# Kernel optimization log

Hardware: AMD Instinct MI355X
Metric: run time of the kernel (lower is better)

## Reference

```python
import jax, jax.numpy as jnp
import numpy as np

B = 8
RESOLUTIONS = [65, 129, 257, 513, 1025]
NUM_POINTS = [0, 4096, 16384, 65536, 262144]
CLIP_MIN = -1e9
FINAL = 1025          # last resolution (both axes)
B_MIN, B_MAX = -1.0, 1.0
BALANCE = 0.5


def setup_inputs() -> dict:
    key = jax.random.key(0)
    k1, k2, k3, k4 = jax.random.split(key, 4)
    return {
        "w1": jax.random.normal(k1, (2, 256), jnp.float32),
        "b1": jax.random.normal(k2, (256,), jnp.float32),
        "w2": jax.random.normal(k3, (256, 1), jnp.float32),
        "b2": jax.random.normal(k4, (1,), jnp.float32),
    }


def _interp_bilinear_ac(x, H, W):
    """F.interpolate(..., mode='bilinear', align_corners=True). x: [B, C, h, w]."""
    b, c, h, w = x.shape
    ys = jnp.linspace(0.0, h - 1.0, H)
    xs = jnp.linspace(0.0, w - 1.0, W)
    y0 = jnp.floor(ys).astype(jnp.int32)
    y1 = jnp.minimum(y0 + 1, h - 1)
    wy = ys - y0
    x0 = jnp.floor(xs).astype(jnp.int32)
    x1 = jnp.minimum(x0 + 1, w - 1)
    wx = xs - x0
    # interpolate rows, then columns
    top = x[:, :, y0, :] * (1.0 - wy)[None, None, :, None] + x[:, :, y1, :] * wy[None, None, :, None]
    return top[:, :, :, x0] * (1.0 - wx) + top[:, :, :, x1] * wx


def _batch_eval(coords, w1, b1, w2, b2):
    """coords: [B, N, 2] in final-resolution pixel space (align_corners=False mapping).
    Returns occupancy [B, N] (C == 1)."""
    coords2d = coords / FINAL + 0.5 / FINAL                 # normalize to [0, 1]
    p = coords2d * (B_MAX - B_MIN) + B_MIN                  # [B, N, 2] in world coords
    h = jax.nn.relu(jnp.einsum('bnd,dh->bnh', p, w1) + b1)  # [B, N, 256]
    occ = jax.nn.sigmoid(jnp.einsum('bnh,ho->bno', h, w2) + b2)
    return occ[..., 0]


def reference(w1, b1, w2, b2):
    occ = None
    for i, res in enumerate(RESOLUTIONS):
        if i == 0:
            # init_coords: grid of res x res points spanning [0, FINAL-1]
            xs = jnp.linspace(0.0, FINAL - 1.0, res)
            gy, gx = jnp.meshgrid(xs, xs, indexing='ij')          # y rows, x cols
            coords = jnp.stack([gx.ravel(), gy.ravel()], axis=-1)  # [N, 2] (x, y)
            coords = jnp.broadcast_to(coords, (B, res * res, 2))
            o = _batch_eval(coords, w1, b1, w2, b2)               # [B, N]
            occ = o.reshape(B, 1, res, res)                       # [B, C, H, W]
        else:
            occ = _interp_bilinear_ac(occ, res, res)
            npt = NUM_POINTS[i]
            if npt <= 0:
                continue
            # uncertainty = -|occ - balance_value|
            unc = -jnp.abs(occ - BALANCE)                          # [B, 1, H, W]
            flat_unc = unc.reshape(B, res * res)
            scores, idx = jax.lax.top_k(flat_unc, npt)             # [B, npt]
            px = (idx % res).astype(jnp.float32)
            py = (idx // res).astype(jnp.float32)
            stride = (FINAL - 1.0) / (res - 1.0)
            coords = jnp.stack([px, py], axis=-1) * stride         # [B, npt, 2]
            new_vals = _batch_eval(coords, w1, b1, w2, b2)         # [B, npt]
            occ_flat = occ.reshape(B, res * res)
            old_vals = jnp.take_along_axis(occ_flat, idx, axis=1)
            vals = jnp.where(scores >= CLIP_MIN, new_vals, old_vals)
            occ_flat = jax.vmap(lambda o, i2, v: o.at[i2].set(v))(occ_flat, idx, vals)
            occ = occ_flat.reshape(B, 1, res, res)
    return occ
```

## Files before the change

kernel.cpp:

```cpp
#include <hip/hip_runtime.h>
#include <stdint.h>

#define HID 256
#define NMAXPIX (1025 * 1025)
#define NREP 8
#define NSEG 2048
#define SELMAX 2112

#define HISTA_OFF 0
#define HISTB_OFF 16384
#define HISTC_OFF 32768
#define SCAL_OFF  40960
#define TIC_OFF   41024
#define STAGE_U32 43072

#define R1P 65
#define R1  129
#define N1  (129 * 129)
#define NPT1 4096u
#define NSEG1 256
#define SEG1 66
#define B1 64
#define NREP1 4

__device__ __forceinline__ uint32_t aload(const uint32_t* p) {
    return __hip_atomic_load(p, __ATOMIC_RELAXED, __HIP_MEMORY_SCOPE_AGENT);
}
__device__ __forceinline__ void astore(uint32_t* p, uint32_t v) {
    __hip_atomic_store(p, v, __ATOMIC_RELAXED, __HIP_MEMORY_SCOPE_AGENT);
}

__device__ __forceinline__ float mlp_eval4(float wx, float wy,
                                           const float4* __restrict__ w1x,
                                           const float4* __restrict__ w1y,
                                           const float4* __restrict__ vb1,
                                           const float4* __restrict__ vw2, float b2v) {
    const float C0 = (float)(0.5 / 1025.0);
    float px = (wx / 1025.0f + C0) * 2.0f - 1.0f;
    float py = (wy / 1025.0f + C0) * 2.0f - 1.0f;
    float a0 = 0.f, a1 = 0.f, a2 = 0.f, a3 = 0.f;
#pragma unroll 8
    for (int q = 0; q < HID / 4; ++q) {
        float4 a = w1x[q], b = w1y[q], c = vb1[q], d = vw2[q];
        float h0 = px * a.x + py * b.x + c.x;
        float h1 = px * a.y + py * b.y + c.y;
        float h2 = px * a.z + py * b.z + c.z;
        float h3 = px * a.w + py * b.w + c.w;
        h0 = h0 > 0.f ? h0 : 0.f;
        h1 = h1 > 0.f ? h1 : 0.f;
        h2 = h2 > 0.f ? h2 : 0.f;
        h3 = h3 > 0.f ? h3 : 0.f;
        a0 += h0 * d.x;
        a1 += h1 * d.y;
        a2 += h2 * d.z;
        a3 += h3 * d.w;
    }
    float x = ((a0 + a1) + (a2 + a3)) + b2v;
    float r;
    if (x >= 0.f) { r = 1.0f / (1.0f + expf(-x)); }
    else { float e = expf(x); r = e / (1.0f + e); }
    return r;
}

__device__ __forceinline__ uint32_t block_exscan_256(uint32_t v, volatile uint32_t* lds4) {
    int lane = threadIdx.x & 63, w = threadIdx.x >> 6;
    uint32_t inc = v;
#pragma unroll
    for (int d = 1; d < 64; d <<= 1) {
        uint32_t o = (uint32_t)__shfl_up((int)inc, d, 64);
        if (lane >= d) inc += o;
    }
    if (lane == 63) lds4[w] = inc;
    __syncthreads();
    uint32_t woff = 0;
    for (int i = 0; i < w; ++i) woff += lds4[i];
    return woff + inc - v;
}

__device__ void scan_generic(const uint32_t* __restrict__ hist, int NB, int nrep,
                             uint32_t rem_in, uint32_t prefix_in, int shift,
                             uint32_t* outp, uint32_t* outr,
                             volatile uint32_t* lds4, volatile uint32_t* ldspair) {
    int tid = threadIdx.x;
    int C = NB >> 8;
    int b0 = NB - (tid + 1) * C;
    uint32_t cnts[8];
#pragma unroll
    for (int k = 0; k < 8; ++k) cnts[k] = 0;
    for (int rep = 0; rep < nrep; ++rep) {
        const uint4* p = (const uint4*)(hist + (size_t)rep * NB + b0);
#pragma unroll
        for (int g = 0; g < 2; ++g) {
            if (g * 4 < C) {
                uint4 v = p[g];
                cnts[g * 4 + 0] += v.x;
                cnts[g * 4 + 1] += v.y;
                cnts[g * 4 + 2] += v.z;
                cnts[g * 4 + 3] += v.w;
            }
        }
    }
    uint32_t ssum = 0;
    for (int k = 0; k < C; ++k) ssum += cnts[k];
    uint32_t excl = block_exscan_256(ssum, lds4);
    uint32_t run = excl;
    for (int k = 0; k < C; ++k) {
        uint32_t c = cnts[C - 1 - k];
        if (rem_in > run && rem_in <= run + c) {
            ldspair[0] = (prefix_in << shift) | (uint32_t)(b0 + C - 1 - k);
            ldspair[1] = rem_in - run;
        }
        run += c;
    }
    __syncthreads();
    *outp = ldspair[0];
    *outr = ldspair[1];
}

__device__ void scan_atomic(const uint32_t* __restrict__ hist, int NB, int nrep,
                            uint32_t rem_in, uint32_t prefix_in, int shift,
                            uint32_t* outp, uint32_t* outr,
                            volatile uint32_t* lds4, volatile uint32_t* ldspair) {
    int tid = threadIdx.x;
    int C = NB >> 8;
    int b0 = NB - (tid + 1) * C;
    uint32_t cnts[8];
#pragma unroll
    for (int k = 0; k < 8; ++k) cnts[k] = 0;
    for (int rep = 0; rep < nrep; ++rep)
        for (int k = 0; k < C; ++k)
            cnts[k] += aload(&hist[(size_t)rep * NB + b0 + k]);
    uint32_t ssum = 0;
    for (int k = 0; k < C; ++k) ssum += cnts[k];
    uint32_t excl = block_exscan_256(ssum, lds4);
    uint32_t run = excl;
    for (int k = 0; k < C; ++k) {
        uint32_t c = cnts[C - 1 - k];
        if (rem_in > run && rem_in <= run + c) {
            ldspair[0] = (prefix_in << shift) | (uint32_t)(b0 + C - 1 - k);
            ldspair[1] = rem_in - run;
        }
        run += c;
    }
    __syncthreads();
    *outp = ldspair[0];
    *outr = ldspair[1];
}

__device__ __forceinline__ void hist_add(uint32_t* lh, uint32_t bin, bool act, int lane) {
    unsigned long long m = __ballot(act);
    if (m) {
        int leader = __ffsll(m) - 1;
        uint32_t lbin = (uint32_t)__shfl((int)bin, leader, 64);
        unsigned long long smk = __ballot(act && bin == lbin);
        if (smk == m) {
            if (lane == leader) atomicAdd(&lh[lbin], (uint32_t)__popcll(m));
        } else if (act) {
            atomicAdd(&lh[bin], 1u);
        }
    }
}

__device__ __forceinline__ float up2x(const float* __restrict__ in, int rp, int r, int n) {
    int i = n / r, j = n % r;
    int i2 = i >> 1, j2 = j >> 1;
    float v;
    if ((i & 1) == 0) {
        if ((j & 1) == 0) {
            v = in[i2 * rp + j2];
        } else {
            float a = in[i2 * rp + j2], b = in[i2 * rp + j2 + 1];
            v = a * 0.5f + b * 0.5f;
        }
    } else {
        if ((j & 1) == 0) {
            float a = in[i2 * rp + j2], b = in[(i2 + 1) * rp + j2];
            v = a * 0.5f + b * 0.5f;
        } else {
            float a = in[i2 * rp + j2],      c = in[i2 * rp + j2 + 1];
            float b = in[(i2 + 1) * rp + j2], d = in[(i2 + 1) * rp + j2 + 1];
            float t1 = a * 0.5f + b * 0.5f;
            float t2 = c * 0.5f + d * 0.5f;
            v = t1 * 0.5f + t2 * 0.5f;
        }
    }
    return v;
}

__device__ __forceinline__ uint32_t mkkey(float v) {
    float unc = -fabsf(v - 0.5f);
    uint32_t u = __float_as_uint(unc);
    return (u & 0x80000000u) ? ~u : (u | 0x80000000u);
}

__device__ __forceinline__ uint32_t key_of(const float* __restrict__ in, int rp, int r, int n) {
    return mkkey(up2x(in, rp, r, n));
}

__device__ bool wait_ctr(uint32_t* ctr, uint32_t target, volatile uint32_t* sflag) {
    if (threadIdx.x == 0) {
        uint32_t d = aload(ctr);
        int sp = 0;
        while (d < target && sp < 20000) {
            __builtin_amdgcn_s_sleep(4);
            d = aload(ctr);
            ++sp;
        }
        *sflag = (d >= target) ? 1u : 0u;
    }
    __syncthreads();
    return *sflag != 0;
}

__global__ __launch_bounds__(256) void k_eval0z(const float* __restrict__ w1, const float* __restrict__ b1,
                                                const float* __restrict__ w2, const float* __restrict__ b2,
                                                float* __restrict__ occ, uint32_t* __restrict__ zbuf, int zcount) {
    __shared__ alignas(16) float sw1[2 * HID];
    __shared__ alignas(16) float sb1[HID];
    __shared__ alignas(16) float sw2[HID];
    int tid = threadIdx.x;
    for (int i = tid; i < 2 * HID; i += 256) sw1[i] = w1[i];
    sb1[tid] = b1[tid];
    sw2[tid] = w2[tid];
    __syncthreads();
    int gtid = blockIdx.x * 256 + tid;
    int nthreads = gridDim.x * 256;
    for (int i = gtid; i < zcount; i += nthreads) zbuf[i] = 0;
    for (int n = gtid; n < 65 * 65; n += nthreads) {
        int i = n / 65, j = n % 65;
        occ[n] = mlp_eval4(16.0f * (float)j, 16.0f * (float)i,
                           (const float4*)sw1, (const float4*)(sw1 + HID),
                           (const float4*)sb1, (const float4*)sw2, b2[0]);
    }
}

__global__ __launch_bounds__(256) void k_s1all(const float* __restrict__ in,
                                               float* __restrict__ outg,
                                               uint32_t* __restrict__ keys,
                                               uint32_t* __restrict__ sm,
                                               const float* __restrict__ w1, const float* __restrict__ b1,
                                               const float* __restrict__ w2, const float* __restrict__ b2) {
    __shared__ alignas(16) float sw1[2 * HID];
    __shared__ alignas(16) float sb1[HID];
    __shared__ alignas(16) float sw2[HID];
    __shared__ alignas(16) uint32_t lh[2048];
    __shared__ uint32_t selidx[SELMAX];
    __shared__ uint32_t selcnt;
    __shared__ uint32_t lds4[4];
    __shared__ uint32_t ldspair[2];
    __shared__ uint32_t sflag;

    uint32_t* histA = sm + HISTA_OFF;
    uint32_t* histB = sm + HISTB_OFF;
    uint32_t* histC = sm + HISTC_OFF;
    uint32_t* scal  = sm + SCAL_OFF;
    uint32_t* tic   = sm + TIC_OFF;

    const int tid = threadIdx.x, lane = tid & 63, w = tid >> 6;
    for (int i = tid; i < 2 * HID; i += 256) sw1[i] = w1[i];
    sb1[tid] = b1[tid];
    sw2[tid] = w2[tid];
    if (tid == 0) selcnt = 0;
    for (int k = tid; k < 2048; k += 256) lh[k] = 0;
    __syncthreads();

    for (int n0 = blockIdx.x * 256; n0 < N1; n0 += B1 * 256) {
        int n = n0 + tid;
        bool act = n < N1;
        uint32_t key = 0;
        if (act) {
            float v = up2x(in, R1P, R1, n);
            outg[n] = v;
            key = mkkey(v);
            astore(&keys[n], key);
        }
        hist_add(lh, key >> 21, act, lane);
    }
    __syncthreads();
    {
        uint32_t* rep = histA + (size_t)(blockIdx.x & (NREP1 - 1)) * 2048;
        for (int k = tid; k < 2048; k += 256) { uint32_t c = lh[k]; if (c) atomicAdd(&rep[k], c); }
    }
    __syncthreads();
    if (tid == 0) __hip_atomic_fetch_add(&scal[8], 1u, __ATOMIC_RELAXED, __HIP_MEMORY_SCOPE_AGENT);

    uint32_t pfx1, rem1;
    if (wait_ctr(&scal[8], B1, &sflag)) {
        scan_atomic(histA, 2048, NREP1, NPT1, 0u, 0, &pfx1, &rem1, lds4, ldspair);
    } else {
        for (int k = tid; k < 2048; k += 256) lh[k] = 0;
        __syncthreads();
        for (int n0 = 0; n0 < N1; n0 += 256) {
            int n = n0 + tid; bool act = n < N1;
            uint32_t key = act ? key_of(in, R1P, R1, n) : 0u;
            hist_add(lh, key >> 21, act, lane);
        }
        __syncthreads();
        scan_generic(lh, 2048, 1, NPT1, 0u, 0, &pfx1, &rem1, lds4, ldspair);
    }

    for (int k = tid; k < 2048; k += 256) lh[k] = 0;
    __syncthreads();
    for (int n0 = blockIdx.x * 256; n0 < N1; n0 += B1 * 256) {
        int n = n0 + tid;
        bool act = n < N1;
        uint32_t key = act ? aload(&keys[n]) : 0u;
        bool flt = act && ((key >> 21) == pfx1);
        hist_add(lh, (key >> 10) & 0x7FFu, flt, lane);
    }
    __syncthreads();
    {
        uint32_t* rep = histB + (size_t)(blockIdx.x & (NREP1 - 1)) * 2048;
        for (int k = tid; k < 2048; k += 256) { uint32_t c = lh[k]; if (c) atomicAdd(&rep[k], c); }
    }
    __syncthreads();
    if (tid == 0) __hip_atomic_fetch_add(&scal[9], 1u, __ATOMIC_RELAXED, __HIP_MEMORY_SCOPE_AGENT);

    uint32_t pfx2, rem2;
    if (wait_ctr(&scal[9], B1, &sflag)) {
        scan_atomic(histB, 2048, NREP1, rem1, pfx1, 11, &pfx2, &rem2, lds4, ldspair);
    } else {
        for (int k = tid; k < 2048; k += 256) lh[k] = 0;
        __syncthreads();
        for (int n0 = 0; n0 < N1; n0 += 256) {
            int n = n0 + tid; bool act = n < N1;
            uint32_t key = act ? key_of(in, R1P, R1, n) : 0u;
            bool flt = act && ((key >> 21) == pfx1);
            hist_add(lh, (key >> 10) & 0x7FFu, flt, lane);
        }
        __syncthreads();
        scan_generic(lh, 2048, 1, rem1, pfx1, 11, &pfx2, &rem2, lds4, ldspair);
    }

    for (int k = tid; k < 2048; k += 256) lh[k] = 0;
    __syncthreads();
    for (int n0 = blockIdx.x * 256; n0 < N1; n0 += B1 * 256) {
        int n = n0 + tid;
        bool act = n < N1;
        uint32_t key = act ? aload(&keys[n]) : 0u;
        bool flt = act && ((key >> 10) == pfx2);
        hist_add(lh, key & 0x3FFu, flt, lane);
    }
    __syncthreads();
    {
        uint32_t* rep = histC + (size_t)(blockIdx.x & (NREP1 - 1)) * 1024;
        for (int k = tid; k < 1024; k += 256) { uint32_t c = lh[k]; if (c) atomicAdd(&rep[k], c); }
    }
    __syncthreads();
    if (tid == 0) __hip_atomic_fetch_add(&scal[10], 1u, __ATOMIC_RELAXED, __HIP_MEMORY_SCOPE_AGENT);

    uint32_t K, t;
    if (wait_ctr(&scal[10], B1, &sflag)) {
        scan_atomic(histC, 1024, NREP1, rem2, pfx2, 10, &K, &t, lds4, ldspair);
    } else {
        for (int k = tid; k < 2048; k += 256) lh[k] = 0;
        __syncthreads();
        for (int n0 = 0; n0 < N1; n0 += 256) {
            int n = n0 + tid; bool act = n < N1;
            uint32_t key = act ? key_of(in, R1P, R1, n) : 0u;
            bool flt = act && ((key >> 10) == pfx2);
            hist_add(lh, key & 0x3FFu, flt, lane);
        }
        __syncthreads();
        scan_generic(lh, 1024, 1, rem2, pfx2, 10, &K, &t, lds4, ldspair);
    }

    int wv = blockIdx.x * 4 + w;
    int s0 = wv * SEG1;
    int s1e = s0 + SEG1; if (s1e > N1) s1e = N1;
    uint32_t tcnt = 0;
    for (int base = s0; base < s1e; base += 64) {
        int n = base + lane;
        if (n < s1e) tcnt += (aload(&keys[n]) == K) ? 1u : 0u;
    }
#pragma unroll
    for (int d = 32; d; d >>= 1) tcnt += (uint32_t)__shfl_down((int)tcnt, d, 64);
    if (lane == 0) astore(&tic[wv], tcnt);
    __syncthreads();
    if (tid == 0) __hip_atomic_fetch_add(&scal[11], 1u, __ATOMIC_RELAXED, __HIP_MEMORY_SCOPE_AGENT);

    uint32_t tp = 0;
    if (wait_ctr(&scal[11], B1, &sflag)) {
        for (int i = lane; i < wv; i += 64) tp += aload(&tic[i]);
    } else {
        for (int i = lane; i < wv; i += 64) {
            int a0 = i * SEG1, a1 = a0 + SEG1; if (a1 > N1) a1 = N1;
            uint32_t c = 0;
            for (int n2 = a0; n2 < a1; ++n2) c += (key_of(in, R1P, R1, n2) == K) ? 1u : 0u;
            tp += c;
        }
    }
#pragma unroll
    for (int d = 32; d; d >>= 1) tp += (uint32_t)__shfl_down((int)tp, d, 64);
    tp = (uint32_t)__shfl((int)tp, 0, 64);

    uint32_t tie_run = tp;
    unsigned long long lowmask = (lane == 63) ? ~0ull >> 1 : ((1ull << lane) - 1ull);
    for (int base = s0; base < s1e; base += 64) {
        int n = base + lane;
        bool inb = n < s1e;
        uint32_t key = inb ? aload(&keys[n]) : 0u;
        bool gt = inb && (key > K);
        bool tie = inb && (key == K);
        unsigned long long tm = __ballot(tie);
        uint32_t trank = tie_run + (uint32_t)__popcll(tm & lowmask);
        bool sel = gt || (tie && trank < t);
        unsigned long long smk = __ballot(sel);
        if (smk) {
            int leader = __ffsll(smk) - 1;
            uint32_t wbase = 0;
            if (lane == leader) wbase = atomicAdd(&selcnt, (uint32_t)__popcll(smk));
            wbase = (uint32_t)__shfl((int)wbase, leader, 64);
            if (sel) selidx[wbase + (uint32_t)__popcll(smk & lowmask)] = (uint32_t)n;
        }
        tie_run += (uint32_t)__popcll(tm);
    }
    __syncthreads();

    uint32_t cnt = selcnt;
    float vb2 = b2[0];
    for (uint32_t i = tid; i < cnt; i += 256) {
        int n = (int)selidx[i];
        int ii = n / R1, jj = n % R1;
        float rr = mlp_eval4(8.0f * (float)jj, 8.0f * (float)ii,
                             (const float4*)sw1, (const float4*)(sw1 + HID),
                             (const float4*)sb1, (const float4*)sw2, vb2);
        outg[n] = rr;
    }
}

__global__ __launch_bounds__(256) void k_upkey(const float* __restrict__ in, int rp,
                                               float* __restrict__ outg, int r, int nb, int bstride,
                                               uint32_t* __restrict__ keys,
                                               uint32_t* __restrict__ histA) {
    __shared__ uint32_t hist[2048];
    int tid = threadIdx.x;
    for (int k = tid; k < 2048; k += 256) hist[k] = 0;
    __syncthreads();
    int N = r * r;
    int lane = tid & 63;
    int gstride = gridDim.x * 256;
    for (int n0 = blockIdx.x * 256; n0 < N; n0 += gstride) {
        int n = n0 + tid;
        bool act = n < N;
        uint32_t key = 0;
        if (act) {
            float v = up2x(in, rp, r, n);
            for (int k = 0; k < nb; ++k) outg[(size_t)k * bstride + n] = v;
            key = mkkey(v);
            keys[n] = key;
        }
        hist_add(hist, key >> 21, act, lane);
    }
    __syncthreads();
    uint32_t* myrep = histA + (size_t)(blockIdx.x & (NREP - 1)) * 2048;
    for (int k = tid; k < 2048; k += 256) {
        uint32_t c = hist[k];
        if (c) atomicAdd(&myrep[k], c);
    }
}

__global__ __launch_bounds__(256) void k_histmid(const uint32_t* __restrict__ keys, int N,
                                                 const uint32_t* __restrict__ prevHist,
                                                 uint32_t* __restrict__ scal,
                                                 int useNpt, uint32_t npt, int scalInIdx, int shift,
                                                 int scalOutIdx,
                                                 int fshift, int bshift, uint32_t bmask,
                                                 uint32_t* __restrict__ outHist, int NBout) {
    __shared__ uint32_t lh[2048];
    __shared__ uint32_t lds4[4];
    __shared__ uint32_t ldspair[2];
    int tid = threadIdx.x, lane = tid & 63;
    uint32_t rem_in = useNpt ? npt : scal[scalInIdx + 1];
    uint32_t pfx_in = useNpt ? 0u  : scal[scalInIdx];
    uint32_t pfx, rem;
    scan_generic(prevHist, 2048, NREP, rem_in, pfx_in, shift, &pfx, &rem, lds4, ldspair);
    if (blockIdx.x == 0 && tid == 0) { scal[scalOutIdx] = pfx; scal[scalOutIdx + 1] = rem; }
    for (int k = tid; k < 2048; k += 256) lh[k] = 0;
    __syncthreads();
    int gstride = gridDim.x * 256;
    for (int base = blockIdx.x * 256; base < N; base += gstride) {
        int n = base + tid;
        bool inb = n < N;
        uint32_t key = inb ? keys[n] : 0u;
        bool flt = inb && ((key >> fshift) == pfx);
        uint32_t bin = (key >> bshift) & bmask;
        hist_add(lh, bin, flt, lane);
    }
    __syncthreads();
    uint32_t* myrep = outHist + (size_t)(blockIdx.x & (NREP - 1)) * NBout;
    for (int k = tid; k < NBout; k += 256) {
        uint32_t c = lh[k];
        if (c) atomicAdd(&myrep[k], c);
    }
}

__global__ __launch_bounds__(256, 2) void k_segselc(
        const uint32_t* __restrict__ keys, int N, int seglen,
        const uint32_t* __restrict__ histC,
        const uint32_t* __restrict__ scal,
        uint32_t* __restrict__ tic,
        uint32_t* __restrict__ gcnt,
        uint32_t* __restrict__ selbuf) {
    __shared__ uint32_t selcnt;
    __shared__ uint32_t selidx[SELMAX];
    __shared__ uint32_t lds4[4];
    __shared__ uint32_t ldspair[2];
    __shared__ uint32_t wtc[4];
    __shared__ uint32_t s_excl;
    __shared__ uint32_t gbase;
    int tid = threadIdx.x, lane = tid & 63, w = tid >> 6;
    if (tid == 0) { selcnt = 0; s_excl = 0; }

    uint32_t rem2 = scal[3], pfx2 = scal[2];
    uint32_t K, t;
    scan_generic(histC, 1024, NREP, rem2, pfx2, 10, &K, &t, lds4, ldspair);

    int wv = blockIdx.x * 4 + w;
    int s0 = wv * seglen;
    int s1 = s0 + seglen; if (s1 > N) s1 = N;
    uint32_t tcnt = 0;
    for (int base = s0; base < s1; base += 64) {
        int n = base + lane;
        if (n < s1) tcnt += (keys[n] == K) ? 1u : 0u;
    }
#pragma unroll
    for (int d = 32; d; d >>= 1) tcnt += (uint32_t)__shfl_down((int)tcnt, d, 64);
    if (lane == 0) wtc[w] = tcnt;
    __syncthreads();
    uint32_t agg = wtc[0] + wtc[1] + wtc[2] + wtc[3];
    uint32_t intra = 0;
    for (int i = 0; i < w; ++i) intra += wtc[i];

    if (tid == 0) {
        uint32_t st = (blockIdx.x == 0) ? ((2u << 30) | agg) : ((1u << 30) | agg);
        astore(&tic[blockIdx.x], st);
    }
    if (blockIdx.x > 0 && w == 0) {
        uint32_t excl = 0;
        int b = (int)blockIdx.x - 1;
        for (;;) {
            int mine = b - lane;
            bool active = (mine >= 0);
            uint32_t f = 0;
            if (active) {
                f = aload(&tic[mine]);
                int spins = 0;
                while ((f >> 30) == 0u && spins < 1000) {
                    __builtin_amdgcn_s_sleep(2);
                    f = aload(&tic[mine]);
                    ++spins;
                }
                if ((f >> 30) == 0u) {
                    int ms0 = mine * seglen;
                    int ms1 = ms0 + seglen; if (ms1 > N) ms1 = N;
                    uint32_t c = 0;
                    for (int n2 = ms0; n2 < ms1; ++n2) c += (keys[n2] == K) ? 1u : 0u;
                    f = (1u << 30) | c;
                }
            }
            unsigned long long incm = __ballot(active && (f >> 30) == 2u);
            uint32_t val;
            bool done = (incm != 0ull);
            if (done) {
                int l2 = __ffsll(incm) - 1;
                val = (lane <= l2) ? (f & 0x3FFFFFFFu) : 0u;
            } else {
                val = active ? (f & 0x3FFFFFFFu) : 0u;
            }
#pragma unroll
            for (int d = 32; d; d >>= 1) val += (uint32_t)__shfl_down((int)val, d, 64);
            val = (uint32_t)__shfl((int)val, 0, 64);
            excl += val;
            if (done) break;
            if (b < 64) break;
            b -= 64;
        }
        if (lane == 0) {
            astore(&tic[blockIdx.x], (2u << 30) | (excl + agg));
            s_excl = excl;
        }
    }
    __syncthreads();
    uint32_t tie_run = s_excl + intra;

    unsigned long long lowmask = (lane == 63) ? ~0ull >> 1 : ((1ull << lane) - 1ull);
    for (int base = s0; base < s1; base += 64) {
        int n = base + lane;
        bool inb = n < s1;
        uint32_t key = inb ? keys[n] : 0u;
        bool gt = inb && (key > K);
        bool tie = inb && (key == K);
        unsigned long long tm = __ballot(tie);
        uint32_t trank = tie_run + (uint32_t)__popcll(tm & lowmask);
        bool sel = gt || (tie && trank < t);
        unsigned long long smk = __ballot(sel);
        if (smk) {
            int leader = __ffsll(smk) - 1;
            uint32_t wbase = 0;
            if (lane == leader) wbase = atomicAdd(&selcnt, (uint32_t)__popcll(smk));
            wbase = (uint32_t)__shfl((int)wbase, leader, 64);
            if (sel) selidx[wbase + (uint32_t)__popcll(smk & lowmask)] = (uint32_t)n;
        }
        tie_run += (uint32_t)__popcll(tm);
    }
    __syncthreads();

    if (tid == 0) gbase = atomicAdd(gcnt, selcnt);
    __syncthreads();
    uint32_t cnt = selcnt, gb = gbase;
    for (uint32_t i = tid; i < cnt; i += 256) selbuf[gb + i] = selidx[i];
}

__global__ __launch_bounds__(256) void k_evalsel(const uint32_t* __restrict__ selbuf, int npt,
                                                 int r, float stride,
                                                 float* __restrict__ occ, int nb, int bstride,
                                                 const float* __restrict__ w1, const float* __restrict__ b1,
                                                 const float* __restrict__ w2, const float* __restrict__ b2) {
    __shared__ alignas(16) float sw1[2 * HID];
    __shared__ alignas(16) float sb1[HID];
    __shared__ alignas(16) float sw2[HID];
    int tid = threadIdx.x;
    for (int i = tid; i < 2 * HID; i += 256) sw1[i] = w1[i];
    sb1[tid] = b1[tid];
    sw2[tid] = w2[tid];
    __syncthreads();
    float vb2 = b2[0];
    int gs = gridDim.x * 256;
    for (int i = blockIdx.x * 256 + tid; i < npt; i += gs) {
        int n = (int)selbuf[i];
        int ii = n / r, jj = n % r;
        float rr = mlp_eval4(stride * (float)jj, stride * (float)ii,
                             (const float4*)sw1, (const float4*)(sw1 + HID),
                             (const float4*)sb1, (const float4*)sw2, vb2);
        for (int k = 0; k < nb; ++k) occ[(size_t)k * bstride + n] = rr;
    }
}

__global__ __launch_bounds__(256) void k_bcast(const float* __restrict__ src, float* __restrict__ dst, int N) {
    int q = blockIdx.x * 256 + threadIdx.x;
    int n = q * 4;
    if (n + 3 < N) {
        float4 v = *(const float4*)(src + n);
#pragma unroll
        for (int k = 0; k < 8; ++k) *(float4*)(dst + (size_t)k * N + n) = v;
    } else if (n < N) {
        for (int m = n; m < N; ++m) {
            float v = src[m];
#pragma unroll
            for (int k = 0; k < 8; ++k) dst[(size_t)k * N + m] = v;
        }
    }
}

extern "C" void kernel_launch(void* const* d_in, const int* in_sizes, int n_in,
                              void* d_out, int out_size, void* d_ws, size_t ws_size,
                              hipStream_t stream) {
    const float* w1 = (const float*)d_in[0];
    const float* b1 = (const float*)d_in[1];
    const float* w2 = (const float*)d_in[2];
    const float* b2 = (const float*)d_in[3];
    float* out = (float*)d_out;

    const size_t A = (((size_t)NMAXPIX * 4) + 255) & ~(size_t)255;
    const size_t SMALL_BYTES = (size_t)4 * STAGE_U32 * 4;
    const size_t SELB_BYTES = ((size_t)262144 * 4 + 255) & ~(size_t)255;
    const size_t need = 3 * A + SMALL_BYTES + SELB_BYTES;

    int fused8 = (ws_size >= need);
    char* base = fused8 ? (char*)d_ws : (char*)d_out;
    float* buf0 = (float*)(base);
    float* buf1 = (float*)(base + A);
    uint32_t* keys = (uint32_t*)(base + 2 * A);
    uint32_t* smallb = (uint32_t*)(base + 3 * A);
    uint32_t* selbuf = (uint32_t*)(base + 3 * A + SMALL_BYTES);

    k_eval0z<<<dim3(512), dim3(256), 0, stream>>>(w1, b1, w2, b2, buf0, smallb, 4 * STAGE_U32);

    k_s1all<<<dim3(B1), dim3(256), 0, stream>>>(buf0, buf1, keys, smallb, w1, b1, w2, b2);

    const int resA[5] = {65, 129, 257, 513, 1025};
    const int nptA[5] = {0, 4096, 16384, 65536, 262144};
    float* cur = buf1;
    float* nxt = buf0;
    for (int s = 2; s < 5; ++s) {
        int rp = resA[s - 1], r = resA[s];
        int N = r * r;
        uint32_t npt = (uint32_t)nptA[s];
        uint32_t* sm    = smallb + (size_t)(s - 1) * STAGE_U32;
        uint32_t* histA = sm + HISTA_OFF;
        uint32_t* histB = sm + HISTB_OFF;
        uint32_t* histC = sm + HISTC_OFF;
        uint32_t* scal  = sm + SCAL_OFF;
        uint32_t* tic   = sm + TIC_OFF;
        int nb1 = (N + 255) / 256;
        int nbu = nb1 < 1024 ? nb1 : 1024;
        int seglen = (N + NSEG - 1) / NSEG;
        float stride = 1024.0f / (float)(r - 1);

        int last = (s == 4);
        float* stage_out = (last && fused8) ? out : nxt;
        int nb = (last && fused8) ? 8 : 1;
        int bstride = (last && fused8) ? NMAXPIX : 0;

        int nbe = (int)((npt + 255) / 256); if (nbe > 512) nbe = 512;

        k_upkey<<<dim3(nbu), dim3(256), 0, stream>>>(cur, rp, stage_out, r, nb, bstride, keys, histA);
        k_histmid<<<dim3(512), dim3(256), 0, stream>>>(keys, N, histA, scal, 1, npt, 0, 0,
                                                       0, 21, 10, 0x7FFu, histB, 2048);
        k_histmid<<<dim3(512), dim3(256), 0, stream>>>(keys, N, histB, scal, 0, 0u, 0, 11,
                                                       2, 10, 0, 0x3FFu, histC, 1024);
        k_segselc<<<dim3(NSEG / 4), dim3(256), 0, stream>>>(keys, N, seglen, histC, scal, tic,
                                                            scal + 6, selbuf);
        k_evalsel<<<dim3(nbe), dim3(256), 0, stream>>>(selbuf, (int)npt, r, stride,
                                                       stage_out, nb, bstride, w1, b1, w2, b2);
        if (!(last && fused8)) { float* tmp = cur; cur = nxt; nxt = tmp; }
    }
    if (!fused8) {
        k_bcast<<<dim3(((NMAXPIX + 3) / 4 + 255) / 256), dim3(256), 0, stream>>>(cur, out, NMAXPIX);
    }
}
```

Before: 240.6 us.

## Fuse two radix histogram passes into one kernel with per-block flag barrier

Merges the two k_histmid launches into a single k_hist12 kernel that builds histB, then waits on a grid-wide barrier made of per-block flags before building histC. This saves one kernel launch per stage. The stage-1 fused kernel's counter-based waits are also replaced by per-block flag stores that one wavefront sweeps, to avoid contention on a single atomic counter. If the flag spin times out, each block falls back to recomputing the histogram on its own, and the barrier relies on all 512 blocks being resident at once.

After: 290.1 us. 1.21x slower.

```diff
diff --git a/kernel.cpp b/kernel.cpp
--- a/kernel.cpp
+++ b/kernel.cpp
@@ -18,10 +18,10 @@
 #define R1  129
 #define N1  (129 * 129)
 #define NPT1 4096u
-#define NSEG1 256
 #define SEG1 66
 #define B1 64
 #define NREP1 4
+#define S1F(e) (1024 + 64 * (e))
 
 __device__ __forceinline__ uint32_t aload(const uint32_t* p) {
     return __hip_atomic_load(p, __ATOMIC_RELAXED, __HIP_MEMORY_SCOPE_AGENT);
@@ -197,16 +197,26 @@
     return mkkey(up2x(in, rp, r, n));
 }
 
-__device__ bool wait_ctr(uint32_t* ctr, uint32_t target, volatile uint32_t* sflag) {
-    if (threadIdx.x == 0) {
-        uint32_t d = aload(ctr);
-        int sp = 0;
-        while (d < target && sp < 20000) {
-            __builtin_amdgcn_s_sleep(4);
-            d = aload(ctr);
-            ++sp;
-        }
-        *sflag = (d >= target) ? 1u : 0u;
+__device__ bool sweep_flags(const uint32_t* flags, int nflags, volatile uint32_t* sflag,
+                            int spincap) {
+    int tid = threadIdx.x, lane = tid & 63;
+    if (tid < 64) {
+        uint32_t ok = 1;
+        for (int base = 0; base < nflags; base += 64) {
+            int idx = base + lane;
+            if (idx < nflags) {
+                uint32_t f = aload(&flags[idx]);
+                int sp = 0;
+                while (!f && sp < spincap) {
+                    __builtin_amdgcn_s_sleep(2);
+                    f = aload(&flags[idx]);
+                    ++sp;
+                }
+                if (!f) ok = 0;
+            }
+        }
+        unsigned long long bad = __ballot(ok == 0);
+        if (lane == 0) *sflag = (bad == 0ull) ? 1u : 0u;
     }
     __syncthreads();
     return *sflag != 0;
@@ -253,7 +263,6 @@
     uint32_t* histA = sm + HISTA_OFF;
     uint32_t* histB = sm + HISTB_OFF;
     uint32_t* histC = sm + HISTC_OFF;
-    uint32_t* scal  = sm + SCAL_OFF;
     uint32_t* tic   = sm + TIC_OFF;
 
     const int tid = threadIdx.x, lane = tid & 63, w = tid >> 6;
@@ -282,10 +291,10 @@
         for (int k = tid; k < 2048; k += 256) { uint32_t c = lh[k]; if (c) atomicAdd(&rep[k], c); }
     }
     __syncthreads();
-    if (tid == 0) __hip_atomic_fetch_add(&scal[8], 1u, __ATOMIC_RELAXED, __HIP_MEMORY_SCOPE_AGENT);
+    if (tid == 0) astore(&tic[S1F(0) + blockIdx.x], 1u);
 
     uint32_t pfx1, rem1;
-    if (wait_ctr(&scal[8], B1, &sflag)) {
+    if (sweep_flags(&tic[S1F(0)], B1, &sflag, 4000)) {
         scan_atomic(histA, 2048, NREP1, NPT1, 0u, 0, &pfx1, &rem1, lds4, ldspair);
     } else {
         for (int k = tid; k < 2048; k += 256) lh[k] = 0;
@@ -314,10 +323,10 @@
         for (int k = tid; k < 2048; k += 256) { uint32_t c = lh[k]; if (c) atomicAdd(&rep[k], c); }
     }
     __syncthreads();
-    if (tid == 0) __hip_atomic_fetch_add(&scal[9], 1u, __ATOMIC_RELAXED, __HIP_MEMORY_SCOPE_AGENT);
+    if (tid == 0) astore(&tic[S1F(1) + blockIdx.x], 1u);
 
     uint32_t pfx2, rem2;
-    if (wait_ctr(&scal[9], B1, &sflag)) {
+    if (sweep_flags(&tic[S1F(1)], B1, &sflag, 4000)) {
         scan_atomic(histB, 2048, NREP1, rem1, pfx1, 11, &pfx2, &rem2, lds4, ldspair);
     } else {
         for (int k = tid; k < 2048; k += 256) lh[k] = 0;
@@ -347,10 +356,10 @@
         for (int k = tid; k < 1024; k += 256) { uint32_t c = lh[k]; if (c) atomicAdd(&rep[k], c); }
     }
     __syncthreads();
-    if (tid == 0) __hip_atomic_fetch_add(&scal[10], 1u, __ATOMIC_RELAXED, __HIP_MEMORY_SCOPE_AGENT);
+    if (tid == 0) astore(&tic[S1F(2) + blockIdx.x], 1u);
 
     uint32_t K, t;
-    if (wait_ctr(&scal[10], B1, &sflag)) {
+    if (sweep_flags(&tic[S1F(2)], B1, &sflag, 4000)) {
         scan_atomic(histC, 1024, NREP1, rem2, pfx2, 10, &K, &t, lds4, ldspair);
     } else {
         for (int k = tid; k < 2048; k += 256) lh[k] = 0;
@@ -377,10 +386,10 @@
     for (int d = 32; d; d >>= 1) tcnt += (uint32_t)__shfl_down((int)tcnt, d, 64);
     if (lane == 0) astore(&tic[wv], tcnt);
     __syncthreads();
-    if (tid == 0) __hip_atomic_fetch_add(&scal[11], 1u, __ATOMIC_RELAXED, __HIP_MEMORY_SCOPE_AGENT);
+    if (tid == 0) astore(&tic[S1F(3) + blockIdx.x], 1u);
 
     uint32_t tp = 0;
-    if (wait_ctr(&scal[11], B1, &sflag)) {
+    if (sweep_flags(&tic[S1F(3)], B1, &sflag, 4000)) {
         for (int i = lane; i < wv; i += 64) tp += aload(&tic[i]);
     } else {
         for (int i = lane; i < wv; i += 64) {
@@ -460,38 +469,69 @@
     }
 }
 
-__global__ __launch_bounds__(256) void k_histmid(const uint32_t* __restrict__ keys, int N,
-                                                 const uint32_t* __restrict__ prevHist,
-                                                 uint32_t* __restrict__ scal,
-                                                 int useNpt, uint32_t npt, int scalInIdx, int shift,
-                                                 int scalOutIdx,
-                                                 int fshift, int bshift, uint32_t bmask,
-                                                 uint32_t* __restrict__ outHist, int NBout) {
+__global__ __launch_bounds__(256) void k_hist12(const uint32_t* __restrict__ keys, int N, uint32_t npt,
+                                                const uint32_t* __restrict__ histA,
+                                                uint32_t* __restrict__ scal,
+                                                uint32_t* __restrict__ histB,
+                                                uint32_t* __restrict__ histC,
+                                                uint32_t* __restrict__ flags) {
     __shared__ uint32_t lh[2048];
     __shared__ uint32_t lds4[4];
     __shared__ uint32_t ldspair[2];
+    __shared__ uint32_t sflag;
     int tid = threadIdx.x, lane = tid & 63;
-    uint32_t rem_in = useNpt ? npt : scal[scalInIdx + 1];
-    uint32_t pfx_in = useNpt ? 0u  : scal[scalInIdx];
-    uint32_t pfx, rem;
-    scan_generic(prevHist, 2048, NREP, rem_in, pfx_in, shift, &pfx, &rem, lds4, ldspair);
-    if (blockIdx.x == 0 && tid == 0) { scal[scalOutIdx] = pfx; scal[scalOutIdx + 1] = rem; }
+    int gstride = gridDim.x * 256;
+
+    uint32_t pfx1, rem1;
+    scan_generic(histA, 2048, NREP, npt, 0u, 0, &pfx1, &rem1, lds4, ldspair);
+
     for (int k = tid; k < 2048; k += 256) lh[k] = 0;
     __syncthreads();
-    int gstride = gridDim.x * 256;
     for (int base = blockIdx.x * 256; base < N; base += gstride) {
         int n = base + tid;
         bool inb = n < N;
         uint32_t key = inb ? keys[n] : 0u;
-        bool flt = inb && ((key >> fshift) == pfx);
-        uint32_t bin = (key >> bshift) & bmask;
-        hist_add(lh, bin, flt, lane);
-    }
-    __syncthreads();
-    uint32_t* myrep = outHist + (size_t)(blockIdx.x & (NREP - 1)) * NBout;
-    for (int k = tid; k < NBout; k += 256) {
-        uint32_t c = lh[k];
-        if (c) atomicAdd(&myrep[k], c);
+        bool flt = inb && ((key >> 21) == pfx1);
+        hist_add(lh, (key >> 10) & 0x7FFu, flt, lane);
+    }
+    __syncthreads();
+    {
+        uint32_t* rep = histB + (size_t)(blockIdx.x & (NREP - 1)) * 2048;
+        for (int k = tid; k < 2048; k += 256) { uint32_t c = lh[k]; if (c) atomicAdd(&rep[k], c); }
+    }
+    __syncthreads();
+    if (tid == 0) astore(&flags[blockIdx.x], 1u);
+
+    uint32_t pfx2, rem2;
+    if (sweep_flags(flags, gridDim.x, &sflag, 4000)) {
+        scan_atomic(histB, 2048, NREP, rem1, pfx1, 11, &pfx2, &rem2, lds4, ldspair);
+    } else {
+        for (int k = tid; k < 2048; k += 256) lh[k] = 0;
+        __syncthreads();
+        for (int n0 = 0; n0 < N; n0 += 256) {
+            int n = n0 + tid; bool inb = n < N;
+            uint32_t key = inb ? keys[n] : 0u;
+            bool flt = inb && ((key >> 21) == pfx1);
+            hist_add(lh, (key >> 10) & 0x7FFu, flt, lane);
+        }
+        __syncthreads();
+        scan_generic(lh, 2048, 1, rem1, pfx1, 11, &pfx2, &rem2, lds4, ldspair);
+    }
+    if (blockIdx.x == 0 && tid == 0) { scal[2] = pfx2; scal[3] = rem2; }
+
+    for (int k = tid; k < 2048; k += 256) lh[k] = 0;
+    __syncthreads();
+    for (int base = blockIdx.x * 256; base < N; base += gstride) {
+        int n = base + tid;
+        bool inb = n < N;
+        uint32_t key = inb ? keys[n] : 0u;
+        bool flt = inb && ((key >> 10) == pfx2);
+        hist_add(lh, key & 0x3FFu, flt, lane);
+    }
+    __syncthreads();
+    {
+        uint32_t* rep = histC + (size_t)(blockIdx.x & (NREP - 1)) * 1024;
+        for (int k = tid; k < 1024; k += 256) { uint32_t c = lh[k]; if (c) atomicAdd(&rep[k], c); }
     }
 }
 
@@ -706,10 +746,8 @@
         int nbe = (int)((npt + 255) / 256); if (nbe > 512) nbe = 512;
 
         k_upkey<<<dim3(nbu), dim3(256), 0, stream>>>(cur, rp, stage_out, r, nb, bstride, keys, histA);
-        k_histmid<<<dim3(512), dim3(256), 0, stream>>>(keys, N, histA, scal, 1, npt, 0, 0,
-                                                       0, 21, 10, 0x7FFu, histB, 2048);
-        k_histmid<<<dim3(512), dim3(256), 0, stream>>>(keys, N, histB, scal, 0, 0u, 0, 11,
-                                                       2, 10, 0, 0x3FFu, histC, 1024);
+        k_hist12<<<dim3(512), dim3(256), 0, stream>>>(keys, N, npt, histA, scal,
+                                                      histB, histC, tic + 512);
         k_segselc<<<dim3(NSEG / 4), dim3(256), 0, stream>>>(keys, N, seglen, histC, scal, tic,
                                                             scal + 6, selbuf);
         k_evalsel<<<dim3(nbe), dim3(256), 0, stream>>>(selbuf, (int)npt, r, stride,
```
